# Performance work log

Measured on AMD Instinct MI355X. Metric: run time of the kernel, lower is better.

Reference implementation:

```python
import jax, jax.numpy as jnp
import numpy as np
from jax import lax

B, C, H, W = 16, 128, 128, 128
C8, C16 = C // 8, C // 16
LN_EPS = 1e-5


def dct_mat(N):
    # torch_dct.dct (norm=None): X_k = 2 * sum_n x_n cos(pi*(2n+1)k/(2N))
    n = jnp.arange(N, dtype=jnp.float32)
    k = jnp.arange(N, dtype=jnp.float32)
    return 2.0 * jnp.cos(jnp.pi * (2.0 * n[None, :] + 1.0) * k[:, None] / (2.0 * N))


def setup_inputs() -> dict:
    key = jax.random.key(0)
    ks = jax.random.split(key, 20)
    s = 0.05
    return {
        "x": jax.random.normal(ks[0], (B, C, H, W), dtype=jnp.float32),
        # channel attention (1x1 convs acting on GAP -> stored as dense [out,in])
        "ca_w1": jax.random.normal(ks[1], (C8, C), dtype=jnp.float32) * s,
        "ca_b1": jnp.zeros((C8,), jnp.float32),
        "ca_w2": jax.random.normal(ks[2], (C, C8), dtype=jnp.float32) * s,
        "ca_b2": jnp.zeros((C,), jnp.float32),
        # spatial attention 9x9 conv -> 1 channel
        "sa_w": jax.random.normal(ks[3], (1, C, 9, 9), dtype=jnp.float32) * s,
        "sa_b": jnp.zeros((1,), jnp.float32),
        # frequency channel attention MLP
        "fa_w1": jax.random.normal(ks[4], (C8, C), dtype=jnp.float32) * s,
        "fa_b1": jnp.zeros((C8,), jnp.float32),
        "fa_w2": jax.random.normal(ks[5], (C, C8), dtype=jnp.float32) * s,
        "fa_b2": jnp.zeros((C,), jnp.float32),
        # global context block
        "gc_mask_w": jax.random.normal(ks[6], (C,), dtype=jnp.float32) * s,
        "gc_mask_b": jnp.zeros((), jnp.float32),
        "gc_t1_w": jax.random.normal(ks[7], (C16, C), dtype=jnp.float32) * s,
        "gc_t1_b": jnp.zeros((C16,), jnp.float32),
        "gc_ln_g": jnp.ones((C16,), jnp.float32),
        "gc_ln_b": jnp.zeros((C16,), jnp.float32),
        "gc_t2_w": jax.random.normal(ks[8], (C, C16), dtype=jnp.float32) * s,
        "gc_t2_b": jnp.zeros((C,), jnp.float32),
        # branch mixing weights + output 1x1 conv
        "alpha": jnp.ones((4,), jnp.float32),
        "out_w": jax.random.normal(ks[9], (C, C), dtype=jnp.float32) * s,
        "out_b": jnp.zeros((C,), jnp.float32),
    }


def reference(x, ca_w1, ca_b1, ca_w2, ca_b2, sa_w, sa_b,
              fa_w1, fa_b1, fa_w2, fa_b2,
              gc_mask_w, gc_mask_b, gc_t1_w, gc_t1_b, gc_ln_g, gc_ln_b,
              gc_t2_w, gc_t2_b, alpha, out_w, out_b):
    b, c, h, w = x.shape
    # --- channel attention (SE-style) ---
    gap = x.mean(axis=(2, 3))                                   # [B,C]
    hca = jax.nn.relu(gap @ ca_w1.T + ca_b1)
    ca = jax.nn.sigmoid(hca @ ca_w2.T + ca_b2)                  # [B,C]
    ac = x * ca[:, :, None, None]
    # --- spatial attention (9x9 conv -> sigmoid gate) ---
    smap = lax.conv_general_dilated(x, sa_w, (1, 1), ((4, 4), (4, 4)),
                                    dimension_numbers=("NCHW", "OIHW", "NCHW"))
    as_ = jax.nn.sigmoid(smap + sa_b[None, :, None, None]) * x
    # --- frequency channel attention (DCT-II 2d, mean over freq) ---
    Dw = dct_mat(w)
    Dh = dct_mat(h)
    xf = jnp.einsum("bchw,kw->bchk", x, Dw)
    xf = jnp.einsum("bchk,lh->bclk", xf, Dh)                    # [B,C,H,W] freq
    favg = xf.mean(axis=(2, 3))                                 # [B,C]
    hfa = jax.nn.relu(favg @ fa_w1.T + fa_b1)
    fwt = jax.nn.sigmoid(hfa @ fa_w2.T + fa_b2)
    af = x * fwt[:, :, None, None]
    # --- global context block ---
    mask = jnp.einsum("bchw,c->bhw", x, gc_mask_w) + gc_mask_b  # [B,H,W]
    mask = jax.nn.softmax(mask.reshape(b, h * w), axis=-1)      # [B,HW]
    ctx = jnp.einsum("bcp,bp->bc", x.reshape(b, c, h * w), mask)  # [B,C]
    t = ctx @ gc_t1_w.T + gc_t1_b                               # [B,C/16]
    mu = t.mean(axis=-1, keepdims=True)
    var = ((t - mu) ** 2).mean(axis=-1, keepdims=True)
    t = (t - mu) * lax.rsqrt(var + LN_EPS) * gc_ln_g + gc_ln_b
    t = jax.nn.relu(t)
    ctx2 = t @ gc_t2_w.T + gc_t2_b                              # [B,C]
    ag = x + ctx2[:, :, None, None]
    # --- softmax-weighted fusion + output 1x1 conv ---
    wts = jax.nn.softmax(alpha)
    fused = wts[0] * ac + wts[1] * as_ + wts[2] * af + wts[3] * ag
    return jnp.einsum("bchw,oc->bohw", fused, out_w) + out_b[None, :, None, None]
```

## Files before the change

### kernel.cpp

```cpp
#include <hip/hip_runtime.h>
#include <math.h>

#define B_   16
#define C_   128
#define W_   128
#define HW_  16384

#define OFF_SARR 0
#define OFF_GAP  128
#define OFF_FAVG 2176
#define OFF_CTX  4224
#define OFF_G    6272
#define OFF_CB   8320
#define OFF_WTS  10368
#define OFF_M    16384
#define OFF_S    (16384 + 262144)
#define OFF_SMAP (16384 + 2 * 262144)

__device__ __forceinline__ float wave_reduce_sum(float v) {
#pragma unroll
  for (int o = 32; o > 0; o >>= 1) v += __shfl_down(v, o, 64);
  return v;
}

__global__ void k0_sarr(float* __restrict__ sarr) {
  int w = threadIdx.x;
  double a = 3.14159265358979323846 * (2.0 * w + 1.0) / 256.0;
  double s = 0.0;
  for (int k = 0; k < 128; ++k) s += cos(a * (double)k);
  sarr[w] = (float)(2.0 * s);
}

__global__ __launch_bounds__(256) void k1_planered(const float* __restrict__ x,
                                                   const float* __restrict__ sarr,
                                                   float* __restrict__ gap,
                                                   float* __restrict__ favg) {
  __shared__ float sL[128];
  __shared__ float buf[8];
  int tid = threadIdx.x;
  int bc = blockIdx.x;
  if (tid < 128) sL[tid] = sarr[tid];
  __syncthreads();
  const float* xp = x + (size_t)bc * HW_;
  float s0 = 0.f, s1 = 0.f;
  for (int i = tid << 2; i < HW_; i += 1024) {
    float4 v = *(const float4*)(xp + i);
    int y = i >> 7, xs = i & 127;
    float shy = sL[y];
    float d = v.x * sL[xs] + v.y * sL[xs + 1] + v.z * sL[xs + 2] + v.w * sL[xs + 3];
    s0 += v.x + v.y + v.z + v.w;
    s1 += shy * d;
  }
  s0 = wave_reduce_sum(s0);
  s1 = wave_reduce_sum(s1);
  int lane = tid & 63, wv = tid >> 6;
  if (lane == 0) { buf[wv] = s0; buf[4 + wv] = s1; }
  __syncthreads();
  if (tid == 0) {
    gap[bc]  = (buf[0] + buf[1] + buf[2] + buf[3]) * (1.f / 16384.f);
    favg[bc] = (buf[4] + buf[5] + buf[6] + buf[7]) * (1.f / 16384.f);
  }
}

__global__ __launch_bounds__(256) void k2_masklogit(const float* __restrict__ x,
                                                    const float* __restrict__ gcw,
                                                    const float* __restrict__ gcb,
                                                    float* __restrict__ m) {
  __shared__ float gl[128];
  int tid = threadIdx.x;
  int b = blockIdx.x >> 4;
  int chunk = blockIdx.x & 15;
  if (tid < 128) gl[tid] = gcw[tid];
  __syncthreads();
  int p0 = (chunk << 10) + (tid << 2);
  const float* xp = x + (size_t)b * C_ * HW_ + p0;
  float4 acc = make_float4(0.f, 0.f, 0.f, 0.f);
  for (int c = 0; c < 128; ++c) {
    float4 v = *(const float4*)(xp + (size_t)c * HW_);
    float wv = gl[c];
    acc.x = fmaf(wv, v.x, acc.x);
    acc.y = fmaf(wv, v.y, acc.y);
    acc.z = fmaf(wv, v.z, acc.z);
    acc.w = fmaf(wv, v.w, acc.w);
  }
  float bb = gcb[0];
  acc.x += bb; acc.y += bb; acc.z += bb; acc.w += bb;
  *(float4*)(m + b * HW_ + p0) = acc;
}

__global__ __launch_bounds__(256) void k3_softmax(float* __restrict__ m) {
  __shared__ float buf[4];
  int b = blockIdx.x;
  int tid = threadIdx.x;
  float* mb = m + b * HW_;
  float mx = -1e30f;
  for (int i = tid << 2; i < HW_; i += 1024) {
    float4 v = *(const float4*)(mb + i);
    mx = fmaxf(mx, fmaxf(fmaxf(v.x, v.y), fmaxf(v.z, v.w)));
  }
#pragma unroll
  for (int o = 32; o > 0; o >>= 1) mx = fmaxf(mx, __shfl_down(mx, o, 64));
  if ((tid & 63) == 0) buf[tid >> 6] = mx;
  __syncthreads();
  if (tid == 0) buf[0] = fmaxf(fmaxf(buf[0], buf[1]), fmaxf(buf[2], buf[3]));
  __syncthreads();
  mx = buf[0];
  __syncthreads();
  float s = 0.f;
  for (int i = tid << 2; i < HW_; i += 1024) {
    float4 v = *(const float4*)(mb + i);
    float4 e;
    e.x = __expf(v.x - mx); e.y = __expf(v.y - mx);
    e.z = __expf(v.z - mx); e.w = __expf(v.w - mx);
    *(float4*)(mb + i) = e;
    s += e.x + e.y + e.z + e.w;
  }
  s = wave_reduce_sum(s);
  if ((tid & 63) == 0) buf[tid >> 6] = s;
  __syncthreads();
  if (tid == 0) buf[0] = buf[0] + buf[1] + buf[2] + buf[3];
  __syncthreads();
  float inv = 1.f / buf[0];
  for (int i = tid << 2; i < HW_; i += 1024) {
    float4 v = *(const float4*)(mb + i);
    v.x *= inv; v.y *= inv; v.z *= inv; v.w *= inv;
    *(float4*)(mb + i) = v;
  }
}

__global__ __launch_bounds__(256) void k4_ctx(const float* __restrict__ x,
                                              const float* __restrict__ mask,
                                              float* __restrict__ ctx) {
  __shared__ float buf[4];
  int tid = threadIdx.x;
  int bc = blockIdx.x;
  int b = bc >> 7;
  const float* xp = x + (size_t)bc * HW_;
  const float* mp = mask + b * HW_;
  float s = 0.f;
  for (int i = tid << 2; i < HW_; i += 1024) {
    float4 v = *(const float4*)(xp + i);
    float4 mk = *(const float4*)(mp + i);
    s += v.x * mk.x + v.y * mk.y + v.z * mk.z + v.w * mk.w;
  }
  s = wave_reduce_sum(s);
  if ((tid & 63) == 0) buf[tid >> 6] = s;
  __syncthreads();
  if (tid == 0) ctx[bc] = buf[0] + buf[1] + buf[2] + buf[3];
}

__global__ __launch_bounds__(128) void k5_mlp(
    const float* __restrict__ gap, const float* __restrict__ favg,
    const float* __restrict__ ctx,
    const float* __restrict__ ca_w1, const float* __restrict__ ca_b1,
    const float* __restrict__ ca_w2, const float* __restrict__ ca_b2,
    const float* __restrict__ fa_w1, const float* __restrict__ fa_b1,
    const float* __restrict__ fa_w2, const float* __restrict__ fa_b2,
    const float* __restrict__ t1w, const float* __restrict__ t1b,
    const float* __restrict__ lng, const float* __restrict__ lnb,
    const float* __restrict__ t2w, const float* __restrict__ t2b,
    const float* __restrict__ alpha,
    const float* __restrict__ out_w, const float* __restrict__ out_b,
    float* __restrict__ g, float* __restrict__ cb, float* __restrict__ wts) {
  int b = blockIdx.x, t = threadIdx.x;
  __shared__ float gapL[128], favL[128], ctxL[128], hca[16], hfa[16], tl[8], dl[128];
  gapL[t] = gap[(b << 7) + t];
  favL[t] = favg[(b << 7) + t];
  ctxL[t] = ctx[(b << 7) + t];
  __syncthreads();
  if (t < 16) {
    float a = ca_b1[t], f = fa_b1[t];
    for (int c = 0; c < 128; ++c) {
      a += gapL[c] * ca_w1[t * 128 + c];
      f += favL[c] * fa_w1[t * 128 + c];
    }
    hca[t] = fmaxf(a, 0.f);
    hfa[t] = fmaxf(f, 0.f);
  }
  if (t < 8) {
    float v = t1b[t];
    for (int c = 0; c < 128; ++c) v += ctxL[c] * t1w[t * 128 + c];
    tl[t] = v;
  }
  __syncthreads();
  float mu = 0.f;
#pragma unroll
  for (int j = 0; j < 8; ++j) mu += tl[j];
  mu *= 0.125f;
  float var = 0.f;
#pragma unroll
  for (int j = 0; j < 8; ++j) { float d = tl[j] - mu; var += d * d; }
  var *= 0.125f;
  float rs = rsqrtf(var + 1e-5f);
  float a0 = alpha[0], a1 = alpha[1], a2 = alpha[2], a3 = alpha[3];
  float am = fmaxf(fmaxf(a0, a1), fmaxf(a2, a3));
  float e0 = __expf(a0 - am), e1 = __expf(a1 - am), e2 = __expf(a2 - am), e3 = __expf(a3 - am);
  float es = 1.f / (e0 + e1 + e2 + e3);
  float w0 = e0 * es, w1 = e1 * es, w2 = e2 * es, w3 = e3 * es;
  float cav = ca_b2[t], fav = fa_b2[t], c2 = t2b[t];
#pragma unroll
  for (int j = 0; j < 16; ++j) {
    cav += hca[j] * ca_w2[t * 16 + j];
    fav += hfa[j] * fa_w2[t * 16 + j];
  }
#pragma unroll
  for (int j = 0; j < 8; ++j) {
    float tn = fmaxf((tl[j] - mu) * rs * lng[j] + lnb[j], 0.f);
    c2 += tn * t2w[t * 8 + j];
  }
  cav = 1.f / (1.f + __expf(-cav));
  fav = 1.f / (1.f + __expf(-fav));
  g[(b << 7) + t] = w0 * cav + w2 * fav + w3;
  dl[t] = w3 * c2;
  __syncthreads();
  float s = out_b[t];
  for (int c = 0; c < 128; ++c) s += out_w[t * 128 + c] * dl[c];
  cb[(b << 7) + t] = s;
  if (b == 0 && t < 4) wts[t] = (t == 0) ? w0 : (t == 1) ? w1 : (t == 2) ? w2 : w3;
}

__global__ __launch_bounds__(256) void k6_conv(const float* __restrict__ x,
                                               const float* __restrict__ saw,
                                               float* __restrict__ smap_part) {
  __shared__ float tile[40 * 72];
  int tid = threadIdx.x;
  int t = blockIdx.x;
  int b = blockIdx.y;
  int split = blockIdx.z;
  int y0 = (t >> 1) << 5;
  int x0 = (t & 1) << 6;
  int rg = tid >> 4;
  int cg = tid & 15;
  int r0 = rg << 1;
  int px0 = cg << 2;
  float acc0[4] = {0.f, 0.f, 0.f, 0.f};
  float acc1[4] = {0.f, 0.f, 0.f, 0.f};
  const float* xb = x + (size_t)b * C_ * HW_;
  int c_lo = split << 5;
  for (int c = c_lo; c < c_lo + 32; ++c) {
    __syncthreads();
    const float* xc = xb + (size_t)c * HW_;
    for (int idx = tid; idx < 720; idx += 256) {
      int row = idx / 18, c4 = idx % 18;
      int gy = y0 - 4 + row;
      int gx = x0 - 4 + (c4 << 2);
      float4 v = make_float4(0.f, 0.f, 0.f, 0.f);
      if (gy >= 0 && gy < 128 && gx >= 0 && gx < 128)
        v = *(const float4*)(xc + gy * W_ + gx);
      *(float4*)(tile + row * 72 + (c4 << 2)) = v;
    }
    __syncthreads();
    const float* wrow = saw + c * 81;
    float rb[2][12];
    {
      const float* tp = tile + r0 * 72 + px0;
      float4 u0 = *(const float4*)tp, u1 = *(const float4*)(tp + 4), u2 = *(const float4*)(tp + 8);
      rb[0][0] = u0.x; rb[0][1] = u0.y; rb[0][2] = u0.z; rb[0][3] = u0.w;
      rb[0][4] = u1.x; rb[0][5] = u1.y; rb[0][6] = u1.z; rb[0][7] = u1.w;
      rb[0][8] = u2.x; rb[0][9] = u2.y; rb[0][10] = u2.z; rb[0][11] = u2.w;
    }
#pragma unroll
    for (int dy = 0; dy < 9; ++dy) {
      int cur = dy & 1, nxt = cur ^ 1;
      const float* tp = tile + (r0 + dy + 1) * 72 + px0;
      float4 u0 = *(const float4*)tp, u1 = *(const float4*)(tp + 4), u2 = *(const float4*)(tp + 8);
      rb[nxt][0] = u0.x; rb[nxt][1] = u0.y; rb[nxt][2] = u0.z; rb[nxt][3] = u0.w;
      rb[nxt][4] = u1.x; rb[nxt][5] = u1.y; rb[nxt][6] = u1.z; rb[nxt][7] = u1.w;
      rb[nxt][8] = u2.x; rb[nxt][9] = u2.y; rb[nxt][10] = u2.z; rb[nxt][11] = u2.w;
#pragma unroll
      for (int dx = 0; dx < 9; ++dx) {
        float wv = wrow[dy * 9 + dx];
#pragma unroll
        for (int j = 0; j < 4; ++j) {
          acc0[j] = fmaf(wv, rb[cur][dx + j], acc0[j]);
          acc1[j] = fmaf(wv, rb[nxt][dx + j], acc1[j]);
        }
      }
    }
  }
  float* op = smap_part + ((size_t)(split * B_ + b)) * HW_ + (y0 + r0) * W_ + x0 + px0;
  *(float4*)op = make_float4(acc0[0], acc0[1], acc0[2], acc0[3]);
  *(float4*)(op + W_) = make_float4(acc1[0], acc1[1], acc1[2], acc1[3]);
}

__global__ __launch_bounds__(256) void k6b_gate(const float* __restrict__ smap_part,
                                                const float* __restrict__ wts,
                                                const float* __restrict__ sab,
                                                float* __restrict__ s) {
  int i = (blockIdx.x * 256 + threadIdx.x) << 2;
  float w1 = wts[1];
  float bb = sab[0];
  float4 a = *(const float4*)(smap_part + i);
  float4 b4 = *(const float4*)(smap_part + 262144 + i);
  float4 c4 = *(const float4*)(smap_part + 2 * 262144 + i);
  float4 d4 = *(const float4*)(smap_part + 3 * 262144 + i);
  float4 r;
  r.x = w1 / (1.f + __expf(-(a.x + b4.x + c4.x + d4.x + bb)));
  r.y = w1 / (1.f + __expf(-(a.y + b4.y + c4.y + d4.y + bb)));
  r.z = w1 / (1.f + __expf(-(a.z + b4.z + c4.z + d4.z + bb)));
  r.w = w1 / (1.f + __expf(-(a.w + b4.w + c4.w + d4.w + bb)));
  *(float4*)(s + i) = r;
}

__global__ __launch_bounds__(256, 2) void k7_gemm(const float* __restrict__ x,
                                                  const float* __restrict__ w,
                                                  const float* __restrict__ g,
                                                  const float* __restrict__ s,
                                                  const float* __restrict__ cb,
                                                  float* __restrict__ out) {
  __shared__ float wT[64 * 128];
  __shared__ float xm[64 * 128];
  int tid = threadIdx.x;
  int b = blockIdx.x >> 7;
  int pt = blockIdx.x & 127;
  int p0 = pt << 7;
  const float* xb = x + (size_t)b * C_ * HW_ + p0;
  const float* sb = s + b * HW_ + p0;
  int pg = tid & 15, og = tid >> 4;
  int o0 = og << 3;
  int ppA = pg << 2;
  int ppB = 64 + (pg << 2);
  float acc[8][8];
#pragma unroll
  for (int i = 0; i < 8; ++i)
#pragma unroll
    for (int j = 0; j < 8; ++j) acc[i][j] = 0.f;
  int sp4 = (tid & 31) << 2;
  float4 sv = *(const float4*)(sb + sp4);
  int crow = tid >> 5;
  int wc4 = tid & 15;
  int wor = tid >> 4;
  for (int chunk = 0; chunk < 2; ++chunk) {
    int cbase = chunk << 6;
    __syncthreads();
#pragma unroll
    for (int pass = 0; pass < 8; ++pass) {
      int c = cbase + (pass << 3) + crow;
      float4 v = *(const float4*)(xb + (size_t)c * HW_ + sp4);
      float gc = g[(b << 7) + c];
      float4 r;
      r.x = v.x * (gc + sv.x);
      r.y = v.y * (gc + sv.y);
      r.z = v.z * (gc + sv.z);
      r.w = v.w * (gc + sv.w);
      *(float4*)(xm + ((c - cbase) << 7) + sp4) = r;
      int o = (pass << 4) + wor;
      float4 wv = *(const float4*)(w + (o << 7) + cbase + (wc4 << 2));
      int qp = (o >> 2) ^ wc4;
      int ob = o & 3;
      int cl = wc4 << 2;
      wT[(cl + 0) * 128 + (qp << 2) + ob] = wv.x;
      wT[(cl + 1) * 128 + (qp << 2) + ob] = wv.y;
      wT[(cl + 2) * 128 + (qp << 2) + ob] = wv.z;
      wT[(cl + 3) * 128 + (qp << 2) + ob] = wv.w;
    }
    __syncthreads();
#pragma unroll 4
    for (int cl = 0; cl < 64; ++cl) {
      int K = cl >> 2;
      const float* wrow = wT + (cl << 7);
      const float* xrow = xm + (cl << 7);
      float4 wa = *(const float4*)(wrow + ((((og << 1)) ^ K) << 2));
      float4 wb = *(const float4*)(wrow + ((((og << 1) | 1) ^ K) << 2));
      float4 xa = *(const float4*)(xrow + ppA);
      float4 xb4 = *(const float4*)(xrow + ppB);
      float wv[8] = {wa.x, wa.y, wa.z, wa.w, wb.x, wb.y, wb.z, wb.w};
      float xv[8] = {xa.x, xa.y, xa.z, xa.w, xb4.x, xb4.y, xb4.z, xb4.w};
#pragma unroll
      for (int i = 0; i < 8; ++i)
#pragma unroll
        for (int j = 0; j < 8; ++j) acc[i][j] = fmaf(wv[i], xv[j], acc[i][j]);
    }
  }
  size_t obase = ((size_t)((b << 7) + o0)) * HW_ + p0;
#pragma unroll
  for (int i = 0; i < 8; ++i) {
    float cv = cb[(b << 7) + o0 + i];
    float4 r0 = make_float4(acc[i][0] + cv, acc[i][1] + cv, acc[i][2] + cv, acc[i][3] + cv);
    float4 r1 = make_float4(acc[i][4] + cv, acc[i][5] + cv, acc[i][6] + cv, acc[i][7] + cv);
    *(float4*)(out + obase + (size_t)i * HW_ + ppA) = r0;
    *(float4*)(out + obase + (size_t)i * HW_ + ppB) = r1;
  }
}

extern "C" void kernel_launch(void* const* d_in, const int* in_sizes, int n_in,
                              void* d_out, int out_size, void* d_ws, size_t ws_size,
                              hipStream_t stream) {
  const float* x       = (const float*)d_in[0];
  const float* ca_w1   = (const float*)d_in[1];
  const float* ca_b1   = (const float*)d_in[2];
  const float* ca_w2   = (const float*)d_in[3];
  const float* ca_b2   = (const float*)d_in[4];
  const float* sa_w    = (const float*)d_in[5];
  const float* sa_b    = (const float*)d_in[6];
  const float* fa_w1   = (const float*)d_in[7];
  const float* fa_b1   = (const float*)d_in[8];
  const float* fa_w2   = (const float*)d_in[9];
  const float* fa_b2   = (const float*)d_in[10];
  const float* gc_mw   = (const float*)d_in[11];
  const float* gc_mb   = (const float*)d_in[12];
  const float* gc_t1w  = (const float*)d_in[13];
  const float* gc_t1b  = (const float*)d_in[14];
  const float* gc_lng  = (const float*)d_in[15];
  const float* gc_lnb  = (const float*)d_in[16];
  const float* gc_t2w  = (const float*)d_in[17];
  const float* gc_t2b  = (const float*)d_in[18];
  const float* alpha   = (const float*)d_in[19];
  const float* out_w   = (const float*)d_in[20];
  const float* out_b   = (const float*)d_in[21];
  float* out = (float*)d_out;
  float* ws = (float*)d_ws;

  float* sarr = ws + OFF_SARR;
  float* gap  = ws + OFF_GAP;
  float* favg = ws + OFF_FAVG;
  float* ctx  = ws + OFF_CTX;
  float* g    = ws + OFF_G;
  float* cb   = ws + OFF_CB;
  float* wts  = ws + OFF_WTS;
  float* m    = ws + OFF_M;
  float* s    = ws + OFF_S;
  float* smap = ws + OFF_SMAP;

  k0_sarr<<<1, 128, 0, stream>>>(sarr);
  k1_planered<<<2048, 256, 0, stream>>>(x, sarr, gap, favg);
  k2_masklogit<<<256, 256, 0, stream>>>(x, gc_mw, gc_mb, m);
  k3_softmax<<<16, 256, 0, stream>>>(m);
  k4_ctx<<<2048, 256, 0, stream>>>(x, m, ctx);
  k5_mlp<<<16, 128, 0, stream>>>(gap, favg, ctx, ca_w1, ca_b1, ca_w2, ca_b2,
                                 fa_w1, fa_b1, fa_w2, fa_b2, gc_t1w, gc_t1b,
                                 gc_lng, gc_lnb, gc_t2w, gc_t2b, alpha,
                                 out_w, out_b, g, cb, wts);
  k6_conv<<<dim3(8, 16, 4), 256, 0, stream>>>(x, sa_w, smap);
  k6b_gate<<<256, 256, 0, stream>>>(smap, wts, sa_b, s);
  k7_gemm<<<2048, 256, 0, stream>>>(x, out_w, g, s, cb, out);
}
```

Baseline: 587.2 us.

## Split softmax across blocks, double-buffer conv tiles, and widen conv channel split

The per-batch softmax (16 blocks) becomes three kernels: per-1024-chunk max/sum partials, a combine step, and an elementwise normalize over 256 blocks, so more of the GPU is used. The 9x9 conv now double-buffers its shared-memory tile with a padded stride of 76 to overlap loads with compute. When the workspace is large enough it also splits channels 8 ways instead of 4, giving more blocks. The DCT row-sum table is computed with a closed-form expression instead of a loop. The cost is extra launches and extra partial-sum traffic.

```diff
diff --git a/kernel.cpp b/kernel.cpp
--- a/kernel.cpp
+++ b/kernel.cpp
@@ -13,6 +13,10 @@
 #define OFF_G    6272
 #define OFF_CB   8320
 #define OFF_WTS  10368
+#define OFF_PMAX 10496
+#define OFF_PSUM 10752
+#define OFF_SMX  11008
+#define OFF_SINV 11024
 #define OFF_M    16384
 #define OFF_S    (16384 + 262144)
 #define OFF_SMAP (16384 + 2 * 262144)
@@ -24,11 +28,10 @@
 }
 
 __global__ void k0_sarr(float* __restrict__ sarr) {
-  int w = threadIdx.x;
-  double a = 3.14159265358979323846 * (2.0 * w + 1.0) / 256.0;
-  double s = 0.0;
-  for (int k = 0; k < 128; ++k) s += cos(a * (double)k);
-  sarr[w] = (float)(2.0 * s);
+  int n = threadIdx.x;
+  double a = 3.14159265358979323846 * (2.0 * n + 1.0) / 256.0;
+  double v = 2.0 * sin(64.0 * a) * cos(63.5 * a) / sin(0.5 * a);
+  sarr[n] = (float)v;
 }
 
 __global__ __launch_bounds__(256) void k1_planered(const float* __restrict__ x,
@@ -88,44 +91,58 @@
   *(float4*)(m + b * HW_ + p0) = acc;
 }
 
-__global__ __launch_bounds__(256) void k3_softmax(float* __restrict__ m) {
-  __shared__ float buf[4];
-  int b = blockIdx.x;
-  int tid = threadIdx.x;
-  float* mb = m + b * HW_;
-  float mx = -1e30f;
-  for (int i = tid << 2; i < HW_; i += 1024) {
-    float4 v = *(const float4*)(mb + i);
-    mx = fmaxf(mx, fmaxf(fmaxf(v.x, v.y), fmaxf(v.z, v.w)));
-  }
-#pragma unroll
-  for (int o = 32; o > 0; o >>= 1) mx = fmaxf(mx, __shfl_down(mx, o, 64));
-  if ((tid & 63) == 0) buf[tid >> 6] = mx;
-  __syncthreads();
-  if (tid == 0) buf[0] = fmaxf(fmaxf(buf[0], buf[1]), fmaxf(buf[2], buf[3]));
-  __syncthreads();
-  mx = buf[0];
-  __syncthreads();
-  float s = 0.f;
-  for (int i = tid << 2; i < HW_; i += 1024) {
-    float4 v = *(const float4*)(mb + i);
-    float4 e;
-    e.x = __expf(v.x - mx); e.y = __expf(v.y - mx);
-    e.z = __expf(v.z - mx); e.w = __expf(v.w - mx);
-    *(float4*)(mb + i) = e;
-    s += e.x + e.y + e.z + e.w;
-  }
+__global__ __launch_bounds__(256) void k3a_part(const float* __restrict__ m,
+                                                float* __restrict__ pmax,
+                                                float* __restrict__ psum) {
+  __shared__ float buf[8];
+  int blk = blockIdx.x;
+  int tid = threadIdx.x;
+  float4 v = *(const float4*)(m + (blk << 10) + (tid << 2));
+  float mx = fmaxf(fmaxf(v.x, v.y), fmaxf(v.z, v.w));
+#pragma unroll
+  for (int o = 32; o > 0; o >>= 1) mx = fmaxf(mx, __shfl_xor(mx, o, 64));
+  int lane = tid & 63, wv = tid >> 6;
+  if (lane == 0) buf[wv] = mx;
+  __syncthreads();
+  mx = fmaxf(fmaxf(buf[0], buf[1]), fmaxf(buf[2], buf[3]));
+  float s = __expf(v.x - mx) + __expf(v.y - mx) + __expf(v.z - mx) + __expf(v.w - mx);
   s = wave_reduce_sum(s);
-  if ((tid & 63) == 0) buf[tid >> 6] = s;
-  __syncthreads();
-  if (tid == 0) buf[0] = buf[0] + buf[1] + buf[2] + buf[3];
-  __syncthreads();
-  float inv = 1.f / buf[0];
-  for (int i = tid << 2; i < HW_; i += 1024) {
-    float4 v = *(const float4*)(mb + i);
-    v.x *= inv; v.y *= inv; v.z *= inv; v.w *= inv;
-    *(float4*)(mb + i) = v;
-  }
+  if (lane == 0) buf[4 + wv] = s;
+  __syncthreads();
+  if (tid == 0) {
+    pmax[blk] = mx;
+    psum[blk] = buf[4] + buf[5] + buf[6] + buf[7];
+  }
+}
+
+__global__ void k3b_comb(const float* __restrict__ pmax, const float* __restrict__ psum,
+                         float* __restrict__ smx, float* __restrict__ sinv) {
+  int tid = threadIdx.x;
+  int b = tid >> 4, j = tid & 15;
+  float mx = pmax[tid];
+  float sm = psum[tid];
+  float gmx = mx;
+#pragma unroll
+  for (int o = 8; o > 0; o >>= 1) gmx = fmaxf(gmx, __shfl_xor(gmx, o, 64));
+  float e = sm * __expf(mx - gmx);
+#pragma unroll
+  for (int o = 8; o > 0; o >>= 1) e += __shfl_xor(e, o, 64);
+  if (j == 0) { smx[b] = gmx; sinv[b] = 1.f / e; }
+}
+
+__global__ __launch_bounds__(256) void k3c_norm(float* __restrict__ m,
+                                                const float* __restrict__ smx,
+                                                const float* __restrict__ sinv) {
+  int blk = blockIdx.x;
+  int b = blk >> 4;
+  int i = (blk << 10) + (threadIdx.x << 2);
+  float mx = smx[b], inv = sinv[b];
+  float4 v = *(const float4*)(m + i);
+  v.x = __expf(v.x - mx) * inv;
+  v.y = __expf(v.y - mx) * inv;
+  v.z = __expf(v.z - mx) * inv;
+  v.w = __expf(v.w - mx) * inv;
+  *(float4*)(m + i) = v;
 }
 
 __global__ __launch_bounds__(256) void k4_ctx(const float* __restrict__ x,
@@ -219,10 +236,11 @@
   if (b == 0 && t < 4) wts[t] = (t == 0) ? w0 : (t == 1) ? w1 : (t == 2) ? w2 : w3;
 }
 
+template <int CPS>
 __global__ __launch_bounds__(256) void k6_conv(const float* __restrict__ x,
                                                const float* __restrict__ saw,
                                                float* __restrict__ smap_part) {
-  __shared__ float tile[40 * 72];
+  __shared__ float tile[2][40 * 76];
   int tid = threadIdx.x;
   int t = blockIdx.x;
   int b = blockIdx.y;
@@ -236,24 +254,31 @@
   float acc0[4] = {0.f, 0.f, 0.f, 0.f};
   float acc1[4] = {0.f, 0.f, 0.f, 0.f};
   const float* xb = x + (size_t)b * C_ * HW_;
-  int c_lo = split << 5;
-  for (int c = c_lo; c < c_lo + 32; ++c) {
-    __syncthreads();
+  int c_lo = split * CPS;
+
+  auto stage = [&](int bufi, int c) {
     const float* xc = xb + (size_t)c * HW_;
+    float* tb = tile[bufi];
     for (int idx = tid; idx < 720; idx += 256) {
-      int row = idx / 18, c4 = idx % 18;
+      int row = idx / 18, c4 = idx - row * 18;
       int gy = y0 - 4 + row;
       int gx = x0 - 4 + (c4 << 2);
       float4 v = make_float4(0.f, 0.f, 0.f, 0.f);
       if (gy >= 0 && gy < 128 && gx >= 0 && gx < 128)
         v = *(const float4*)(xc + gy * W_ + gx);
-      *(float4*)(tile + row * 72 + (c4 << 2)) = v;
-    }
+      *(float4*)(tb + row * 76 + (c4 << 2)) = v;
+    }
+  };
+
+  stage(0, c_lo);
+  for (int i = 0; i < CPS; ++i) {
     __syncthreads();
-    const float* wrow = saw + c * 81;
+    if (i + 1 < CPS) stage((i + 1) & 1, c_lo + i + 1);
+    const float* tb = tile[i & 1];
+    const float* wrow = saw + (c_lo + i) * 81;
     float rb[2][12];
     {
-      const float* tp = tile + r0 * 72 + px0;
+      const float* tp = tb + r0 * 76 + px0;
       float4 u0 = *(const float4*)tp, u1 = *(const float4*)(tp + 4), u2 = *(const float4*)(tp + 8);
       rb[0][0] = u0.x; rb[0][1] = u0.y; rb[0][2] = u0.z; rb[0][3] = u0.w;
       rb[0][4] = u1.x; rb[0][5] = u1.y; rb[0][6] = u1.z; rb[0][7] = u1.w;
@@ -262,7 +287,7 @@
 #pragma unroll
     for (int dy = 0; dy < 9; ++dy) {
       int cur = dy & 1, nxt = cur ^ 1;
-      const float* tp = tile + (r0 + dy + 1) * 72 + px0;
+      const float* tp = tb + (r0 + dy + 1) * 76 + px0;
       float4 u0 = *(const float4*)tp, u1 = *(const float4*)(tp + 4), u2 = *(const float4*)(tp + 8);
       rb[nxt][0] = u0.x; rb[nxt][1] = u0.y; rb[nxt][2] = u0.z; rb[nxt][3] = u0.w;
       rb[nxt][4] = u1.x; rb[nxt][5] = u1.y; rb[nxt][6] = u1.z; rb[nxt][7] = u1.w;
@@ -283,6 +308,7 @@
   *(float4*)(op + W_) = make_float4(acc1[0], acc1[1], acc1[2], acc1[3]);
 }
 
+template <int NS>
 __global__ __launch_bounds__(256) void k6b_gate(const float* __restrict__ smap_part,
                                                 const float* __restrict__ wts,
                                                 const float* __restrict__ sab,
@@ -291,14 +317,16 @@
   float w1 = wts[1];
   float bb = sab[0];
   float4 a = *(const float4*)(smap_part + i);
-  float4 b4 = *(const float4*)(smap_part + 262144 + i);
-  float4 c4 = *(const float4*)(smap_part + 2 * 262144 + i);
-  float4 d4 = *(const float4*)(smap_part + 3 * 262144 + i);
+#pragma unroll
+  for (int j = 1; j < NS; ++j) {
+    float4 t4 = *(const float4*)(smap_part + (size_t)j * 262144 + i);
+    a.x += t4.x; a.y += t4.y; a.z += t4.z; a.w += t4.w;
+  }
   float4 r;
-  r.x = w1 / (1.f + __expf(-(a.x + b4.x + c4.x + d4.x + bb)));
-  r.y = w1 / (1.f + __expf(-(a.y + b4.y + c4.y + d4.y + bb)));
-  r.z = w1 / (1.f + __expf(-(a.z + b4.z + c4.z + d4.z + bb)));
-  r.w = w1 / (1.f + __expf(-(a.w + b4.w + c4.w + d4.w + bb)));
+  r.x = w1 / (1.f + __expf(-(a.x + bb)));
+  r.y = w1 / (1.f + __expf(-(a.y + bb)));
+  r.z = w1 / (1.f + __expf(-(a.z + bb)));
+  r.w = w1 / (1.f + __expf(-(a.w + bb)));
   *(float4*)(s + i) = r;
 }
 
@@ -418,20 +446,34 @@
   float* g    = ws + OFF_G;
   float* cb   = ws + OFF_CB;
   float* wts  = ws + OFF_WTS;
+  float* pmax = ws + OFF_PMAX;
+  float* psum = ws + OFF_PSUM;
+  float* smx  = ws + OFF_SMX;
+  float* sinv = ws + OFF_SINV;
   float* m    = ws + OFF_M;
   float* s    = ws + OFF_S;
   float* smap = ws + OFF_SMAP;
 
+  size_t need8 = (size_t)(16384 + 10 * 262144) * sizeof(float);
+  int use8 = (ws_size >= need8) ? 1 : 0;
+
   k0_sarr<<<1, 128, 0, stream>>>(sarr);
   k1_planered<<<2048, 256, 0, stream>>>(x, sarr, gap, favg);
   k2_masklogit<<<256, 256, 0, stream>>>(x, gc_mw, gc_mb, m);
-  k3_softmax<<<16, 256, 0, stream>>>(m);
+  k3a_part<<<256, 256, 0, stream>>>(m, pmax, psum);
+  k3b_comb<<<1, 256, 0, stream>>>(pmax, psum, smx, sinv);
+  k3c_norm<<<256, 256, 0, stream>>>(m, smx, sinv);
   k4_ctx<<<2048, 256, 0, stream>>>(x, m, ctx);
   k5_mlp<<<16, 128, 0, stream>>>(gap, favg, ctx, ca_w1, ca_b1, ca_w2, ca_b2,
                                  fa_w1, fa_b1, fa_w2, fa_b2, gc_t1w, gc_t1b,
                                  gc_lng, gc_lnb, gc_t2w, gc_t2b, alpha,
                                  out_w, out_b, g, cb, wts);
-  k6_conv<<<dim3(8, 16, 4), 256, 0, stream>>>(x, sa_w, smap);
-  k6b_gate<<<256, 256, 0, stream>>>(smap, wts, sa_b, s);
+  if (use8) {
+    k6_conv<16><<<dim3(8, 16, 8), 256, 0, stream>>>(x, sa_w, smap);
+    k6b_gate<8><<<256, 256, 0, stream>>>(smap, wts, sa_b, s);
+  } else {
+    k6_conv<32><<<dim3(8, 16, 4), 256, 0, stream>>>(x, sa_w, smap);
+    k6b_gate<4><<<256, 256, 0, stream>>>(smap, wts, sa_b, s);
+  }
   k7_gemm<<<2048, 256, 0, stream>>>(x, out_w, g, s, cb, out);
 }
```

Result: faster. 542.7 us (-7.6%).
